# Kernel optimization log

Measured on AMD Instinct MI355X. Metric: run time of the kernel, lower is better.

The kernel has to match this reference:

```python
import jax, jax.numpy as jnp
import numpy as np

B, S, DIM = 2, 2048, 2048
N_HEADS, N_KV_HEADS = 16, 4
HEAD_DIM = DIM // N_HEADS  # 128
N_REP = N_HEADS // N_KV_HEADS  # 4


def setup_inputs() -> dict:
    key = jax.random.key(0)
    ks = jax.random.split(key, 7)
    x = jax.random.normal(ks[0], (B, S, DIM), dtype=jnp.float32)
    cos = jax.random.uniform(ks[1], (S, HEAD_DIM // 2), dtype=jnp.float32)
    sin = jax.random.uniform(ks[2], (S, HEAD_DIM // 2), dtype=jnp.float32)
    sc = 1.0 / np.sqrt(DIM)
    wq = jax.random.normal(ks[3], (DIM, N_HEADS * HEAD_DIM), dtype=jnp.float32) * sc
    wk = jax.random.normal(ks[4], (DIM, N_KV_HEADS * HEAD_DIM), dtype=jnp.float32) * sc
    wv = jax.random.normal(ks[5], (DIM, N_KV_HEADS * HEAD_DIM), dtype=jnp.float32) * sc
    wo = jax.random.normal(ks[6], (N_HEADS * HEAD_DIM, DIM), dtype=jnp.float32) * sc
    return {"x": x, "cos": cos, "sin": sin, "wq": wq, "wk": wk, "wv": wv, "wo": wo}


def _rope(t, cos, sin):
    # t: [B, S, H, hd]; cos/sin: [S, hd/2] -> broadcast as [1, S, 1, hd/2]
    tr, ti = t[..., ::2], t[..., 1::2]
    c = cos[None, :, None, :]
    s = sin[None, :, None, :]
    out_r = tr * c - ti * s
    out_i = tr * s + ti * c
    # interleave back: stack on new last axis then flatten
    return jnp.stack([out_r, out_i], axis=-1).reshape(t.shape)


def reference(x, cos, sin, wq, wk, wv, wo):
    bsz, seqlen, _ = x.shape
    xq = (x @ wq).reshape(bsz, seqlen, N_HEADS, HEAD_DIM)
    xk = (x @ wk).reshape(bsz, seqlen, N_KV_HEADS, HEAD_DIM)
    xv = (x @ wv).reshape(bsz, seqlen, N_KV_HEADS, HEAD_DIM)
    xq = _rope(xq, cos, sin)
    xk = _rope(xk, cos, sin)
    # GQA: repeat kv heads -> [B, S, H, hd]
    xk = jnp.repeat(xk, N_REP, axis=2)
    xv = jnp.repeat(xv, N_REP, axis=2)
    scale = 1.0 / jnp.sqrt(jnp.asarray(HEAD_DIM, dtype=x.dtype))
    scores = jnp.einsum("bqhd,bkhd->bhqk", xq, xk) * scale
    causal = jnp.tril(jnp.ones((seqlen, seqlen), dtype=bool))
    scores = jnp.where(causal[None, None, :, :], scores, jnp.asarray(-jnp.inf, dtype=scores.dtype))
    attn = jax.nn.softmax(scores, axis=-1)
    out = jnp.einsum("bhqk,bkhd->bqhd", attn, xv)
    out = out.reshape(bsz, seqlen, N_HEADS * HEAD_DIM)
    return out @ wo
```

## Files before the change

### kernel.cpp

```cpp
#include <hip/hip_runtime.h>
#include <stdint.h>

#define SEQ 2048

typedef uint16_t u16;
typedef uint32_t u32;
typedef __attribute__((ext_vector_type(4))) float f32x4;
typedef __attribute__((ext_vector_type(8))) __bf16 bf16x8;
typedef __attribute__((ext_vector_type(4))) __bf16 bf16x4;

__device__ __forceinline__ u16 f2bf(float f) {
    u32 u = __float_as_uint(f);
    u += 0x7FFFu + ((u >> 16) & 1u);
    return (u16)(u >> 16);
}
__device__ __forceinline__ float bf2f(u16 h) {
    return __uint_as_float(((u32)h) << 16);
}
__device__ __forceinline__ void async16(const void* g, void* l) {
    auto gp = (__attribute__((address_space(1))) void*)const_cast<void*>(g);
    auto lp = (__attribute__((address_space(3))) void*)l;
    __builtin_amdgcn_global_load_lds(gp, lp, 16, 0, 0);
}

__global__ __launch_bounds__(256) void convert_bf16(const float* __restrict__ src,
                                                    u16* __restrict__ dst) {
    int i = blockIdx.x * 256 + threadIdx.x;
    float4 v = ((const float4*)src)[i];
    u32 lo = (u32)f2bf(v.x) | ((u32)f2bf(v.y) << 16);
    u32 hi = (u32)f2bf(v.z) | ((u32)f2bf(v.w) << 16);
    ((uint2*)dst)[i] = make_uint2(lo, hi);
}

__global__ __launch_bounds__(256) void tconv_all(const float* __restrict__ wq,
                                                 const float* __restrict__ wk,
                                                 const float* __restrict__ wv,
                                                 const float* __restrict__ wo,
                                                 u16* __restrict__ wqkvT,
                                                 u16* __restrict__ woT) {
    __shared__ float tile[64][65];
    const int bx = blockIdx.x, k0 = blockIdx.y * 64;
    const float* src; u16* dst; int N, n0;
    if (bx < 32)      { src = wq; dst = wqkvT;                        N = 2048; n0 = bx * 64; }
    else if (bx < 40) { src = wk; dst = wqkvT + (size_t)2048 * 2048;  N = 512;  n0 = (bx - 32) * 64; }
    else if (bx < 48) { src = wv; dst = wqkvT + (size_t)2560 * 2048;  N = 512;  n0 = (bx - 40) * 64; }
    else              { src = wo; dst = woT;                          N = 2048; n0 = (bx - 48) * 64; }
    const int tid = threadIdx.x;
#pragma unroll
    for (int p = 0; p < 4; p++) {
        int r = p * 16 + (tid >> 4);
        int c = (tid & 15) * 4;
        float4 v = *(const float4*)&src[(size_t)(k0 + r) * N + n0 + c];
        tile[r][c] = v.x; tile[r][c+1] = v.y; tile[r][c+2] = v.z; tile[r][c+3] = v.w;
    }
    __syncthreads();
#pragma unroll
    for (int p = 0; p < 4; p++) {
        int n = p * 16 + (tid >> 4);
        int kq = (tid & 15) * 4;
        u32 lo = (u32)f2bf(tile[kq+0][n]) | ((u32)f2bf(tile[kq+1][n]) << 16);
        u32 hi = (u32)f2bf(tile[kq+2][n]) | ((u32)f2bf(tile[kq+3][n]) << 16);
        *(uint2*)&dst[(size_t)(n0 + n) * 2048 + k0 + kq] = make_uint2(lo, hi);
    }
}

template <int BN, bool F32OUT>
__global__ __launch_bounds__(512, 2) void gemm256(const u16* __restrict__ A,
                                                  const u16* __restrict__ Bt,
                                                  void* __restrict__ Cv,
                                                  int N, int K, int nbx) {
    constexpr int MF = (BN == 256) ? 8 : 4;
    constexpr int SLOT = 8192 + BN * 32;
    __shared__ u16 lds[4 * SLOT];

    const int nwg = gridDim.x;
    const int q = nwg >> 3, r = nwg & 7;
    const int xcd = blockIdx.x & 7, lid = blockIdx.x >> 3;
    const int wg = (xcd < r ? xcd * (q + 1) : r * (q + 1) + (xcd - r) * q) + lid;
    const int by = wg / nbx, bx = wg - by * nbx;
    const int m0 = by * 256, n0 = bx * BN;

    const int tid = threadIdx.x;
    const int w = tid >> 6, l = tid & 63;
    const int lr = l & 15, quad = l >> 4;
    const int wm = (BN == 256) ? (w >> 2) * 128 : (w >> 1) * 64;
    const int wn = (BN == 256) ? (w & 3) * 64  : (w & 1) * 64;
    const int cs = (quad ^ (lr & 3)) * 8;

    const int rA = w * 32 + (l >> 2);
    const int gA = ((l & 3) ^ (rA & 3)) * 8;
    const u16* aS = A + (size_t)(m0 + rA) * K + gA;
    u16* ldA = lds + (w * 128 + l) * 8;

    const u16* bS;
    u16* ldB;
    if constexpr (BN == 256) {
        bS = Bt + (size_t)(n0 + rA) * K + gA;
        ldB = lds + 8192 + (w * 128 + l) * 8;
    } else {
        const int rB = w * 16 + (l >> 2);
        const int gB = ((l & 3) ^ (rB & 3)) * 8;
        bS = Bt + (size_t)(n0 + rB) * K + gB;
        ldB = lds + 8192 + tid * 8;
    }

    f32x4 acc[MF][4] = {};
    const int nK = K >> 5;

    auto stageA = [&](int kt) {
        u16* d = ldA + (kt & 3) * SLOT;
        const u16* s = aS + (size_t)kt * 32;
        async16(s, d);
        async16(s + (size_t)16 * K, d + 512);
    };
    auto stageB = [&](int kt) {
        u16* d = ldB + (kt & 3) * SLOT;
        const u16* s = bS + (size_t)kt * 32;
        async16(s, d);
        if constexpr (BN == 256) async16(s + (size_t)16 * K, d + 512);
    };

    stageA(0); stageB(0); stageA(1); stageB(1); stageA(2); stageB(2);
    if constexpr (BN == 256)
        asm volatile("s_waitcnt vmcnt(8)" ::: "memory");
    else
        asm volatile("s_waitcnt vmcnt(6)" ::: "memory");
    __builtin_amdgcn_s_barrier();

    for (int kt = 0; kt < nK; ++kt) {
        const u16* As = lds + (kt & 3) * SLOT;
        const u16* Bs = As + 8192;
        const bool pre = (kt + 3 < nK);
        bf16x8 af[MF], bfr[4];
#pragma unroll
        for (int i = 0; i < MF; i++)
            af[i] = *(const bf16x8*)&As[(wm + i * 16 + lr) * 32 + cs];
#pragma unroll
        for (int i = 0; i < 4; i++)
            bfr[i] = *(const bf16x8*)&Bs[(wn + i * 16 + lr) * 32 + cs];
        if (pre) { stageA(kt + 3); stageB(kt + 3); }
        __builtin_amdgcn_s_barrier();
        asm volatile("s_waitcnt lgkmcnt(0)" ::: "memory");
        __builtin_amdgcn_s_setprio(1);
#pragma unroll
        for (int mf = 0; mf < MF; mf++)
#pragma unroll
            for (int nf = 0; nf < 4; nf++)
                acc[mf][nf] = __builtin_amdgcn_mfma_f32_16x16x32_bf16(af[mf], bfr[nf], acc[mf][nf], 0, 0, 0);
        __builtin_amdgcn_s_setprio(0);
        if constexpr (BN == 256) {
            if (kt < nK - 3)       asm volatile("s_waitcnt vmcnt(8)" ::: "memory");
            else if (kt == nK - 3) asm volatile("s_waitcnt vmcnt(4)" ::: "memory");
            else if (kt == nK - 2) asm volatile("s_waitcnt vmcnt(0)" ::: "memory");
        } else {
            if (kt < nK - 3)       asm volatile("s_waitcnt vmcnt(6)" ::: "memory");
            else if (kt == nK - 3) asm volatile("s_waitcnt vmcnt(3)" ::: "memory");
            else if (kt == nK - 2) asm volatile("s_waitcnt vmcnt(0)" ::: "memory");
        }
        if (kt < nK - 1) __builtin_amdgcn_s_barrier();
    }

#pragma unroll
    for (int mf = 0; mf < MF; mf++) {
#pragma unroll
        for (int nf = 0; nf < 4; nf++) {
#pragma unroll
            for (int rr = 0; rr < 4; rr++) {
                size_t row = (size_t)(m0 + wm + mf * 16 + quad * 4 + rr);
                size_t col = (size_t)(n0 + wn + nf * 16 + lr);
                if (F32OUT)
                    ((float*)Cv)[row * (size_t)N + col] = acc[mf][nf][rr];
                else
                    ((u16*)Cv)[row * (size_t)N + col] = f2bf(acc[mf][nf][rr]);
            }
        }
    }
}

__global__ __launch_bounds__(256) void rope_k(u16* __restrict__ qkv,
                                              const float* __restrict__ cosp,
                                              const float* __restrict__ sinp) {
    const int t = blockIdx.x;
    const int spos = t & (SEQ - 1);
    const int tid = threadIdx.x;
    u16* row = qkv + (size_t)t * 3072;
    const int col = 2048 + 2 * tid;
    const int ci = tid & 63;
    u32 v = *(u32*)(row + col);
    float tr = bf2f((u16)(v & 0xFFFFu));
    float ti = bf2f((u16)(v >> 16));
    float cs = cosp[spos * 64 + ci];
    float sn = sinp[spos * 64 + ci];
    float orr = tr * cs - ti * sn;
    float oi  = tr * sn + ti * cs;
    *(u32*)(row + col) = (u32)f2bf(orr) | ((u32)f2bf(oi) << 16);
}

__global__ __launch_bounds__(256) void transpose_v(const u16* __restrict__ qkv,
                                                   u16* __restrict__ vt) {
    __shared__ u16 tile[64][65];
    const int bid = blockIdx.x;
    const int dt = bid & 1;
    const int st = (bid >> 1) & 31;
    const int kh = (bid >> 6) & 3;
    const int b  = bid >> 8;
    const int tid = threadIdx.x;
#pragma unroll
    for (int pp = 0; pp < 2; pp++) {
        int r  = pp * 32 + (tid >> 3);
        int c8 = (tid & 7) * 8;
        const u16* src = qkv + (size_t)(b * SEQ + st * 64 + r) * 3072 + 2560 + kh * 128 + dt * 64 + c8;
        uint4 v = *(const uint4*)src;
        tile[r][c8+0] = (u16)(v.x & 0xFFFF); tile[r][c8+1] = (u16)(v.x >> 16);
        tile[r][c8+2] = (u16)(v.y & 0xFFFF); tile[r][c8+3] = (u16)(v.y >> 16);
        tile[r][c8+4] = (u16)(v.z & 0xFFFF); tile[r][c8+5] = (u16)(v.z >> 16);
        tile[r][c8+6] = (u16)(v.w & 0xFFFF); tile[r][c8+7] = (u16)(v.w >> 16);
    }
    __syncthreads();
#pragma unroll
    for (int pp = 0; pp < 2; pp++) {
        int dr = pp * 32 + (tid >> 3);
        int s8 = (tid & 7) * 8;
        uint4 o;
        o.x = (u32)tile[s8+0][dr] | ((u32)tile[s8+1][dr] << 16);
        o.y = (u32)tile[s8+2][dr] | ((u32)tile[s8+3][dr] << 16);
        o.z = (u32)tile[s8+4][dr] | ((u32)tile[s8+5][dr] << 16);
        o.w = (u32)tile[s8+6][dr] | ((u32)tile[s8+7][dr] << 16);
        u16* dst = vt + ((size_t)((b * 4 + kh) * 128 + dt * 64 + dr)) * SEQ + st * 64 + s8;
        *(uint4*)dst = o;
    }
}

__global__ __launch_bounds__(512, 2) void flash_attn(const u16* __restrict__ qkv,
                                                     const u16* __restrict__ vt,
                                                     const float* __restrict__ cosp,
                                                     const float* __restrict__ sinp,
                                                     u16* __restrict__ ob) {
    __shared__ u16 sh[65536];
    const int bidx = blockIdx.x;
    const int xcd   = bidx & 7;
    const int inner = bidx >> 3;
    const int b  = xcd >> 2, kh = xcd & 3;
    const int h  = kh * 4 + (inner & 3);
    const int a  = inner >> 2;
    const int tid = threadIdx.x;
    const int w = tid >> 6, lane = tid & 63;
    const int grp = w >> 2, wl = w & 3;
    const int lr = lane & 15, quad = lane >> 4;
    const float qscale = 0.088388347762f * 1.4426950408889634f;

    u16* base_g = sh + grp * 24576;
    u16* vb  = base_g + 16384;
    u16* lPw = sh + 49152 + w * 2048;

    const int tidg = tid & 255;
    const int krow = tidg >> 4;
    const int kchunk = (tidg & 15) ^ krow;
    const int vrow = tidg >> 3;
    const int vchunk = (tidg & 7) ^ (vrow & 7);
    const u16* kRow = qkv + (size_t)b * SEQ * 3072 + 2048 + kh * 128
                    + (size_t)krow * 3072 + kchunk * 8;
    const u16* vRow = vt + (size_t)(b * 4 + kh) * 128 * SEQ
                    + (size_t)vrow * SEQ + vchunk * 8;

    auto stageK = [&](int kt, int buf) {
        u16* d = base_g + buf * 8192 + tidg * 8;
#pragma unroll
        for (int i = 0; i < 4; i++)
            async16(kRow + (size_t)(kt * 64 + i * 16) * 3072, d + i * 2048);
    };
    auto stageV = [&](int kt) {
        u16* d = vb + tidg * 8;
#pragma unroll
        for (int i = 0; i < 4; i++)
            async16(vRow + (size_t)(i * 32) * SEQ + kt * 64, d + i * 2048);
    };

    float* mO = (float*)sh;
    float* mM = (float*)(sh + 49152);

    for (int p = 0; p < 2; p++) {
        const int qt = p ? (7 - a) : (8 + a);
        const int niters = p ? (8 - a) : (9 + a);
        const int kt0 = grp * niters;

        stageK(kt0, 0);

        bf16x8 qf[2][4];
#pragma unroll
        for (int qi = 0; qi < 2; qi++) {
            const int token = qt * 128 + wl * 32 + qi * 16 + lr;
            const u16* qb = qkv + (size_t)(b * SEQ + token) * 3072 + h * 128;
#pragma unroll
            for (int kk = 0; kk < 4; kk++) {
                uint4 raw = *(const uint4*)(qb + kk * 32 + quad * 8);
                u32 rw[4] = {raw.x, raw.y, raw.z, raw.w};
                union { u16 us[8]; bf16x8 v; } fr;
#pragma unroll
                for (int pp = 0; pp < 4; pp++) {
                    int ci = kk * 16 + quad * 4 + pp;
                    float cv = cosp[token * 64 + ci];
                    float sv = sinp[token * 64 + ci];
                    float tr = bf2f((u16)(rw[pp] & 0xFFFFu));
                    float ti = bf2f((u16)(rw[pp] >> 16));
                    fr.us[2 * pp]     = f2bf((tr * cv - ti * sv) * qscale);
                    fr.us[2 * pp + 1] = f2bf((tr * sv + ti * cv) * qscale);
                }
                qf[qi][kk] = fr.v;
            }
        }

        f32x4 o[2][8] = {};
        float m_st[2] = {-1e30f, -1e30f};
        float l_st[2] = {0.f, 0.f};
        const int qg = qt * 128 + wl * 32 + lr;

        for (int t = 0; t < niters; t++) {
            const int kt = kt0 + t;
            const int buf = t & 1;
            stageV(kt);
            if (t + 1 < niters) {
                stageK(kt + 1, buf ^ 1);
                asm volatile("s_waitcnt vmcnt(8)" ::: "memory");
            } else {
                asm volatile("s_waitcnt vmcnt(4)" ::: "memory");
            }
            asm volatile("s_barrier" ::: "memory");

            const u16* kcur = base_g + buf * 8192;
            f32x4 sc[2][4] = {};
            __builtin_amdgcn_s_setprio(1);
#pragma unroll
            for (int nf = 0; nf < 4; nf++) {
#pragma unroll
                for (int kk = 0; kk < 4; kk++) {
                    bf16x8 ak = *(const bf16x8*)&kcur[(nf * 16 + lr) * 128 + (((kk * 4 + quad) ^ lr) * 8)];
                    sc[0][nf] = __builtin_amdgcn_mfma_f32_16x16x32_bf16(ak, qf[0][kk], sc[0][nf], 0, 0, 0);
                    sc[1][nf] = __builtin_amdgcn_mfma_f32_16x16x32_bf16(ak, qf[1][kk], sc[1][nf], 0, 0, 0);
                }
            }
            __builtin_amdgcn_s_setprio(0);

            const int kb = kt * 64 + quad * 4;
            const int kmax = kt * 64 + 63;
#pragma unroll
            for (int qi = 0; qi < 2; qi++) {
                float ps[4][4];
                float tmax = -1e30f;
                const int qrow_g = qg + qi * 16;
                if (kmax > qt * 128 + wl * 32 + qi * 16) {
#pragma unroll
                    for (int nf = 0; nf < 4; nf++)
#pragma unroll
                        for (int r = 0; r < 4; r++) {
                            float v = sc[qi][nf][r];
                            if ((kb + nf * 16 + r) > qrow_g) v = -1e30f;
                            ps[nf][r] = v;
                            tmax = fmaxf(tmax, v);
                        }
                } else {
#pragma unroll
                    for (int nf = 0; nf < 4; nf++)
#pragma unroll
                        for (int r = 0; r < 4; r++) {
                            float v = sc[qi][nf][r];
                            ps[nf][r] = v;
                            tmax = fmaxf(tmax, v);
                        }
                }
                tmax = fmaxf(tmax, __shfl_xor(tmax, 16));
                tmax = fmaxf(tmax, __shfl_xor(tmax, 32));
                const float mprev = m_st[qi];
                if (!__all(tmax - mprev <= 8.0f)) {
                    float mnew = fmaxf(mprev, tmax);
                    float alpha = exp2f(mprev - mnew);
                    l_st[qi] *= alpha;
                    m_st[qi] = mnew;
#pragma unroll
                    for (int r = 0; r < 4; r++) {
                        float ar = __shfl(alpha, quad * 4 + r, 16);
#pragma unroll
                        for (int nd = 0; nd < 8; nd++) o[qi][nd][r] *= ar;
                    }
                }
                const float mcur = m_st[qi];
                float rsum = 0.f;
#pragma unroll
                for (int nf = 0; nf < 4; nf++)
#pragma unroll
                    for (int r = 0; r < 4; r++) {
                        float e = exp2f(ps[nf][r] - mcur);
                        ps[nf][r] = e;
                        rsum += e;
                    }
                rsum += __shfl_xor(rsum, 16);
                rsum += __shfl_xor(rsum, 32);
                l_st[qi] += rsum;
                const int qrow = qi * 16 + lr;
#pragma unroll
                for (int nf = 0; nf < 4; nf++) {
                    u32 lo = (u32)f2bf(ps[nf][0]) | ((u32)f2bf(ps[nf][1]) << 16);
                    u32 hi = (u32)f2bf(ps[nf][2]) | ((u32)f2bf(ps[nf][3]) << 16);
                    int c = (nf * 4 + quad) ^ lr;
                    *(uint2*)&lPw[qrow * 64 + c * 4] = make_uint2(lo, hi);
                }
            }

            if (t + 1 < niters) asm volatile("s_waitcnt vmcnt(4)" ::: "memory");
            else                asm volatile("s_waitcnt vmcnt(0)" ::: "memory");
            asm volatile("s_barrier" ::: "memory");

            __builtin_amdgcn_s_setprio(1);
#pragma unroll
            for (int kf = 0; kf < 2; kf++) {
                bf16x8 pa[2];
#pragma unroll
                for (int qi = 0; qi < 2; qi++) {
                    int c0 = (kf * 8 + quad * 2) ^ lr;
                    int c1 = (kf * 8 + quad * 2 + 1) ^ lr;
                    bf16x4 p0 = *(const bf16x4*)&lPw[(qi * 16 + lr) * 64 + c0 * 4];
                    bf16x4 p1 = *(const bf16x4*)&lPw[(qi * 16 + lr) * 64 + c1 * 4];
                    pa[qi] = __builtin_shufflevector(p0, p1, 0, 1, 2, 3, 4, 5, 6, 7);
                }
#pragma unroll
                for (int nd = 0; nd < 8; nd++) {
                    bf16x8 vv = *(const bf16x8*)&vb[(nd * 16 + lr) * 64 + (((kf * 4 + quad) ^ (lr & 7)) * 8)];
                    o[0][nd] = __builtin_amdgcn_mfma_f32_16x16x32_bf16(pa[0], vv, o[0][nd], 0, 0, 0);
                    o[1][nd] = __builtin_amdgcn_mfma_f32_16x16x32_bf16(pa[1], vv, o[1][nd], 0, 0, 0);
                }
            }
            __builtin_amdgcn_s_setprio(0);

            asm volatile("s_barrier" ::: "memory");
        }

        __syncthreads();
        if (grp == 1) {
#pragma unroll
            for (int qi = 0; qi < 2; qi++) {
#pragma unroll
                for (int r = 0; r < 4; r++) {
                    int row = wl * 32 + qi * 16 + quad * 4 + r;
#pragma unroll
                    for (int nd = 0; nd < 8; nd++)
                        mO[row * 128 + nd * 16 + lr] = o[qi][nd][r];
                }
                if (quad == 0) {
                    int rowl = wl * 32 + qi * 16 + lr;
                    mM[rowl * 2]     = m_st[qi];
                    mM[rowl * 2 + 1] = l_st[qi];
                }
            }
        }
        __syncthreads();
        if (grp == 0) {
#pragma unroll
            for (int qi = 0; qi < 2; qi++) {
                int rowl = wl * 32 + qi * 16 + lr;
                float m1 = mM[rowl * 2], l1 = mM[rowl * 2 + 1];
                float M  = fmaxf(m_st[qi], m1);
                float a0 = exp2f(m_st[qi] - M);
                float a1 = exp2f(m1 - M);
                float li = 1.0f / (l_st[qi] * a0 + l1 * a1);
                u16* obase = ob + (size_t)(b * SEQ + qt * 128 + wl * 32 + qi * 16) * 2048 + h * 128;
#pragma unroll
                for (int r = 0; r < 4; r++) {
                    float a0b = __shfl(a0, quad * 4 + r, 16);
                    float a1b = __shfl(a1, quad * 4 + r, 16);
                    float lib = __shfl(li, quad * 4 + r, 16);
                    int row = wl * 32 + qi * 16 + quad * 4 + r;
#pragma unroll
                    for (int nd = 0; nd < 8; nd++) {
                        float val = (o[qi][nd][r] * a0b + mO[row * 128 + nd * 16 + lr] * a1b) * lib;
                        obase[(quad * 4 + r) * 2048 + nd * 16 + lr] = f2bf(val);
                    }
                }
            }
        }
        __syncthreads();
    }
}

extern "C" void kernel_launch(void* const* d_in, const int* in_sizes, int n_in,
                              void* d_out, int out_size, void* d_ws, size_t ws_size,
                              hipStream_t stream) {
    (void)in_sizes; (void)n_in; (void)out_size; (void)ws_size;
    const float* x    = (const float*)d_in[0];
    const float* cosp = (const float*)d_in[1];
    const float* sinp = (const float*)d_in[2];
    const float* wq   = (const float*)d_in[3];
    const float* wk   = (const float*)d_in[4];
    const float* wv   = (const float*)d_in[5];
    const float* wo   = (const float*)d_in[6];
    float* out = (float*)d_out;

    char* ws = (char*)d_ws;
    u16* xb    = (u16*)(ws);
    u16* qkvb  = (u16*)(ws + (size_t)16 * 1024 * 1024);
    u16* wqkvT = (u16*)(ws + (size_t)40 * 1024 * 1024);
    u16* woT   = (u16*)(ws + (size_t)52 * 1024 * 1024);
    u16* vtb   = (u16*)(ws + (size_t)60 * 1024 * 1024);
    u16* ob    = xb;

    convert_bf16<<<8192, 256, 0, stream>>>(x, xb);
    tconv_all<<<dim3(80, 32), 256, 0, stream>>>(wq, wk, wv, wo, wqkvT, woT);
    gemm256<256, false><<<192, 512, 0, stream>>>(xb, wqkvT, (void*)qkvb, 3072, 2048, 12);
    rope_k<<<4096, 256, 0, stream>>>(qkvb, cosp, sinp);
    transpose_v<<<512, 256, 0, stream>>>(qkvb, vtb);
    flash_attn<<<256, 512, 0, stream>>>(qkvb, vtb, cosp, sinp, ob);
    gemm256<128, true><<<256, 512, 0, stream>>>(ob, woT, (void*)out, 2048, 2048, 16);
}
```

Before: 316.4 us.

## Fuse K RoPE and V transpose into QKV GEMM epilogue, split GEMM k-loop

Removes the separate rope_k and transpose_v kernels. The QKV GEMM epilogue now applies RoPE to the K columns, using a lane shuffle to fetch the pair partner, and writes V directly in transposed layout. The BN=256 GEMM main loop is split into two half-M phases that interleave the A and B prefetch with MFMA work. Manual bf16 rounding is replaced with the packed v_cvt_pk_bf16_f32 instruction, and the softmax max/sum reductions are split into independent chains. This saves two kernel launches and a round trip of K and V through memory, at the cost of extra barriers in the GEMM loop and scattered, uncoalesced global loads of cos/sin in the epilogue.

```diff
diff --git a/kernel.cpp b/kernel.cpp
--- a/kernel.cpp
+++ b/kernel.cpp
@@ -17,6 +17,11 @@
 __device__ __forceinline__ float bf2f(u16 h) {
     return __uint_as_float(((u32)h) << 16);
 }
+__device__ __forceinline__ u32 cvt_pk_bf16(float lo, float hi) {
+    u32 r;
+    asm("v_cvt_pk_bf16_f32 %0, %1, %2" : "=v"(r) : "v"(lo), "v"(hi));
+    return r;
+}
 __device__ __forceinline__ void async16(const void* g, void* l) {
     auto gp = (__attribute__((address_space(1))) void*)const_cast<void*>(g);
     auto lp = (__attribute__((address_space(3))) void*)l;
@@ -27,9 +32,7 @@
                                                     u16* __restrict__ dst) {
     int i = blockIdx.x * 256 + threadIdx.x;
     float4 v = ((const float4*)src)[i];
-    u32 lo = (u32)f2bf(v.x) | ((u32)f2bf(v.y) << 16);
-    u32 hi = (u32)f2bf(v.z) | ((u32)f2bf(v.w) << 16);
-    ((uint2*)dst)[i] = make_uint2(lo, hi);
+    ((uint2*)dst)[i] = make_uint2(cvt_pk_bf16(v.x, v.y), cvt_pk_bf16(v.z, v.w));
 }
 
 __global__ __launch_bounds__(256) void tconv_all(const float* __restrict__ wq,
@@ -58,8 +61,8 @@
     for (int p = 0; p < 4; p++) {
         int n = p * 16 + (tid >> 4);
         int kq = (tid & 15) * 4;
-        u32 lo = (u32)f2bf(tile[kq+0][n]) | ((u32)f2bf(tile[kq+1][n]) << 16);
-        u32 hi = (u32)f2bf(tile[kq+2][n]) | ((u32)f2bf(tile[kq+3][n]) << 16);
+        u32 lo = cvt_pk_bf16(tile[kq+0][n], tile[kq+1][n]);
+        u32 hi = cvt_pk_bf16(tile[kq+2][n], tile[kq+3][n]);
         *(uint2*)&dst[(size_t)(n0 + n) * 2048 + k0 + kq] = make_uint2(lo, hi);
     }
 }
@@ -68,7 +71,10 @@
 __global__ __launch_bounds__(512, 2) void gemm256(const u16* __restrict__ A,
                                                   const u16* __restrict__ Bt,
                                                   void* __restrict__ Cv,
-                                                  int N, int K, int nbx) {
+                                                  int N, int K, int nbx,
+                                                  const float* __restrict__ cosp,
+                                                  const float* __restrict__ sinp,
+                                                  u16* __restrict__ vt) {
     constexpr int MF = (BN == 256) ? 8 : 4;
     constexpr int SLOT = 8192 + BN * 32;
     __shared__ u16 lds[4 * SLOT];
@@ -131,103 +137,129 @@
         const u16* As = lds + (kt & 3) * SLOT;
         const u16* Bs = As + 8192;
         const bool pre = (kt + 3 < nK);
-        bf16x8 af[MF], bfr[4];
-#pragma unroll
-        for (int i = 0; i < MF; i++)
-            af[i] = *(const bf16x8*)&As[(wm + i * 16 + lr) * 32 + cs];
-#pragma unroll
-        for (int i = 0; i < 4; i++)
-            bfr[i] = *(const bf16x8*)&Bs[(wn + i * 16 + lr) * 32 + cs];
-        if (pre) { stageA(kt + 3); stageB(kt + 3); }
-        __builtin_amdgcn_s_barrier();
-        asm volatile("s_waitcnt lgkmcnt(0)" ::: "memory");
-        __builtin_amdgcn_s_setprio(1);
-#pragma unroll
-        for (int mf = 0; mf < MF; mf++)
-#pragma unroll
-            for (int nf = 0; nf < 4; nf++)
-                acc[mf][nf] = __builtin_amdgcn_mfma_f32_16x16x32_bf16(af[mf], bfr[nf], acc[mf][nf], 0, 0, 0);
-        __builtin_amdgcn_s_setprio(0);
         if constexpr (BN == 256) {
+            bf16x8 af[4], bfr[4];
+#pragma unroll
+            for (int i = 0; i < 4; i++)
+                af[i] = *(const bf16x8*)&As[(wm + i * 16 + lr) * 32 + cs];
+#pragma unroll
+            for (int i = 0; i < 4; i++)
+                bfr[i] = *(const bf16x8*)&Bs[(wn + i * 16 + lr) * 32 + cs];
+            if (pre) stageA(kt + 3);
+            __builtin_amdgcn_s_barrier();
+            asm volatile("s_waitcnt lgkmcnt(0)" ::: "memory");
+            __builtin_amdgcn_s_setprio(1);
+#pragma unroll
+            for (int mf = 0; mf < 4; mf++)
+#pragma unroll
+                for (int nf = 0; nf < 4; nf++)
+                    acc[mf][nf] = __builtin_amdgcn_mfma_f32_16x16x32_bf16(af[mf], bfr[nf], acc[mf][nf], 0, 0, 0);
+            __builtin_amdgcn_s_setprio(0);
+            __builtin_amdgcn_s_barrier();
+#pragma unroll
+            for (int i = 0; i < 4; i++)
+                af[i] = *(const bf16x8*)&As[(wm + 64 + i * 16 + lr) * 32 + cs];
+            if (pre) stageB(kt + 3);
+            __builtin_amdgcn_s_barrier();
+            asm volatile("s_waitcnt lgkmcnt(0)" ::: "memory");
+            __builtin_amdgcn_s_setprio(1);
+#pragma unroll
+            for (int mf = 0; mf < 4; mf++)
+#pragma unroll
+                for (int nf = 0; nf < 4; nf++)
+                    acc[4 + mf][nf] = __builtin_amdgcn_mfma_f32_16x16x32_bf16(af[mf], bfr[nf], acc[4 + mf][nf], 0, 0, 0);
+            __builtin_amdgcn_s_setprio(0);
             if (kt < nK - 3)       asm volatile("s_waitcnt vmcnt(8)" ::: "memory");
             else if (kt == nK - 3) asm volatile("s_waitcnt vmcnt(4)" ::: "memory");
             else if (kt == nK - 2) asm volatile("s_waitcnt vmcnt(0)" ::: "memory");
+            if (kt < nK - 1) __builtin_amdgcn_s_barrier();
         } else {
+            bf16x8 af[MF], bfr[4];
+#pragma unroll
+            for (int i = 0; i < MF; i++)
+                af[i] = *(const bf16x8*)&As[(wm + i * 16 + lr) * 32 + cs];
+#pragma unroll
+            for (int i = 0; i < 4; i++)
+                bfr[i] = *(const bf16x8*)&Bs[(wn + i * 16 + lr) * 32 + cs];
+            if (pre) { stageA(kt + 3); stageB(kt + 3); }
+            __builtin_amdgcn_s_barrier();
+            asm volatile("s_waitcnt lgkmcnt(0)" ::: "memory");
+            __builtin_amdgcn_s_setprio(1);
+#pragma unroll
+            for (int mf = 0; mf < MF; mf++)
+#pragma unroll
+                for (int nf = 0; nf < 4; nf++)
+                    acc[mf][nf] = __builtin_amdgcn_mfma_f32_16x16x32_bf16(af[mf], bfr[nf], acc[mf][nf], 0, 0, 0);
+            __builtin_amdgcn_s_setprio(0);
             if (kt < nK - 3)       asm volatile("s_waitcnt vmcnt(6)" ::: "memory");
             else if (kt == nK - 3) asm volatile("s_waitcnt vmcnt(3)" ::: "memory");
             else if (kt == nK - 2) asm volatile("s_waitcnt vmcnt(0)" ::: "memory");
-        }
-        if (kt < nK - 1) __builtin_amdgcn_s_barrier();
-    }
-
-#pragma unroll
-    for (int mf = 0; mf < MF; mf++) {
-#pragma unroll
-        for (int nf = 0; nf < 4; nf++) {
-#pragma unroll
-            for (int rr = 0; rr < 4; rr++) {
-                size_t row = (size_t)(m0 + wm + mf * 16 + quad * 4 + rr);
-                size_t col = (size_t)(n0 + wn + nf * 16 + lr);
-                if (F32OUT)
-                    ((float*)Cv)[row * (size_t)N + col] = acc[mf][nf][rr];
-                else
-                    ((u16*)Cv)[row * (size_t)N + col] = f2bf(acc[mf][nf][rr]);
-            }
+            if (kt < nK - 1) __builtin_amdgcn_s_barrier();
         }
     }
-}
-
-__global__ __launch_bounds__(256) void rope_k(u16* __restrict__ qkv,
-                                              const float* __restrict__ cosp,
-                                              const float* __restrict__ sinp) {
-    const int t = blockIdx.x;
-    const int spos = t & (SEQ - 1);
-    const int tid = threadIdx.x;
-    u16* row = qkv + (size_t)t * 3072;
-    const int col = 2048 + 2 * tid;
-    const int ci = tid & 63;
-    u32 v = *(u32*)(row + col);
-    float tr = bf2f((u16)(v & 0xFFFFu));
-    float ti = bf2f((u16)(v >> 16));
-    float cs = cosp[spos * 64 + ci];
-    float sn = sinp[spos * 64 + ci];
-    float orr = tr * cs - ti * sn;
-    float oi  = tr * sn + ti * cs;
-    *(u32*)(row + col) = (u32)f2bf(orr) | ((u32)f2bf(oi) << 16);
-}
-
-__global__ __launch_bounds__(256) void transpose_v(const u16* __restrict__ qkv,
-                                                   u16* __restrict__ vt) {
-    __shared__ u16 tile[64][65];
-    const int bid = blockIdx.x;
-    const int dt = bid & 1;
-    const int st = (bid >> 1) & 31;
-    const int kh = (bid >> 6) & 3;
-    const int b  = bid >> 8;
-    const int tid = threadIdx.x;
-#pragma unroll
-    for (int pp = 0; pp < 2; pp++) {
-        int r  = pp * 32 + (tid >> 3);
-        int c8 = (tid & 7) * 8;
-        const u16* src = qkv + (size_t)(b * SEQ + st * 64 + r) * 3072 + 2560 + kh * 128 + dt * 64 + c8;
-        uint4 v = *(const uint4*)src;
-        tile[r][c8+0] = (u16)(v.x & 0xFFFF); tile[r][c8+1] = (u16)(v.x >> 16);
-        tile[r][c8+2] = (u16)(v.y & 0xFFFF); tile[r][c8+3] = (u16)(v.y >> 16);
-        tile[r][c8+4] = (u16)(v.z & 0xFFFF); tile[r][c8+5] = (u16)(v.z >> 16);
-        tile[r][c8+6] = (u16)(v.w & 0xFFFF); tile[r][c8+7] = (u16)(v.w >> 16);
-    }
-    __syncthreads();
-#pragma unroll
-    for (int pp = 0; pp < 2; pp++) {
-        int dr = pp * 32 + (tid >> 3);
-        int s8 = (tid & 7) * 8;
-        uint4 o;
-        o.x = (u32)tile[s8+0][dr] | ((u32)tile[s8+1][dr] << 16);
-        o.y = (u32)tile[s8+2][dr] | ((u32)tile[s8+3][dr] << 16);
-        o.z = (u32)tile[s8+4][dr] | ((u32)tile[s8+5][dr] << 16);
-        o.w = (u32)tile[s8+6][dr] | ((u32)tile[s8+7][dr] << 16);
-        u16* dst = vt + ((size_t)((b * 4 + kh) * 128 + dt * 64 + dr)) * SEQ + st * 64 + s8;
-        *(uint4*)dst = o;
+
+    if constexpr (BN == 256 && !F32OUT) {
+        if (n0 >= 2560) {
+            const int bb = m0 >> 11;
+#pragma unroll
+            for (int mf = 0; mf < MF; mf++) {
+                const int token0 = (m0 + wm + mf * 16 + quad * 4) & (SEQ - 1);
+#pragma unroll
+                for (int nf = 0; nf < 4; nf++) {
+                    int dg = n0 - 2560 + wn + nf * 16 + lr;
+                    int kh = dg >> 7, d = dg & 127;
+                    u32 lo = cvt_pk_bf16(acc[mf][nf][0], acc[mf][nf][1]);
+                    u32 hi = cvt_pk_bf16(acc[mf][nf][2], acc[mf][nf][3]);
+                    *(uint2*)&vt[((size_t)((bb * 4 + kh) * 128 + d)) * SEQ + token0] = make_uint2(lo, hi);
+                }
+            }
+        } else if (n0 >= 2048) {
+            const float sgn = (lr & 1) ? 1.0f : -1.0f;
+#pragma unroll
+            for (int mf = 0; mf < MF; mf++) {
+#pragma unroll
+                for (int nf = 0; nf < 4; nf++) {
+                    int col = n0 + wn + nf * 16 + lr;
+                    int ci = (col & 127) >> 1;
+#pragma unroll
+                    for (int rr = 0; rr < 4; rr++) {
+                        size_t row = (size_t)(m0 + wm + mf * 16 + quad * 4 + rr);
+                        int token = (int)row & (SEQ - 1);
+                        float v = acc[mf][nf][rr];
+                        float ppart = __shfl_xor(v, 1);
+                        float c = cosp[token * 64 + ci];
+                        float s = sinp[token * 64 + ci];
+                        float ov = fmaf(sgn * ppart, s, v * c);
+                        ((u16*)Cv)[row * (size_t)N + col] = f2bf(ov);
+                    }
+                }
+            }
+        } else {
+#pragma unroll
+            for (int mf = 0; mf < MF; mf++)
+#pragma unroll
+                for (int nf = 0; nf < 4; nf++)
+#pragma unroll
+                    for (int rr = 0; rr < 4; rr++) {
+                        size_t row = (size_t)(m0 + wm + mf * 16 + quad * 4 + rr);
+                        size_t col = (size_t)(n0 + wn + nf * 16 + lr);
+                        ((u16*)Cv)[row * (size_t)N + col] = f2bf(acc[mf][nf][rr]);
+                    }
+        }
+    } else {
+#pragma unroll
+        for (int mf = 0; mf < MF; mf++)
+#pragma unroll
+            for (int nf = 0; nf < 4; nf++)
+#pragma unroll
+                for (int rr = 0; rr < 4; rr++) {
+                    size_t row = (size_t)(m0 + wm + mf * 16 + quad * 4 + rr);
+                    size_t col = (size_t)(n0 + wn + nf * 16 + lr);
+                    if (F32OUT)
+                        ((float*)Cv)[row * (size_t)N + col] = acc[mf][nf][rr];
+                    else
+                        ((u16*)Cv)[row * (size_t)N + col] = f2bf(acc[mf][nf][rr]);
+                }
     }
 }
 
@@ -295,7 +327,7 @@
             for (int kk = 0; kk < 4; kk++) {
                 uint4 raw = *(const uint4*)(qb + kk * 32 + quad * 8);
                 u32 rw[4] = {raw.x, raw.y, raw.z, raw.w};
-                union { u16 us[8]; bf16x8 v; } fr;
+                union { u32 u[4]; bf16x8 v; } fr;
 #pragma unroll
                 for (int pp = 0; pp < 4; pp++) {
                     int ci = kk * 16 + quad * 4 + pp;
@@ -303,8 +335,8 @@
                     float sv = sinp[token * 64 + ci];
                     float tr = bf2f((u16)(rw[pp] & 0xFFFFu));
                     float ti = bf2f((u16)(rw[pp] >> 16));
-                    fr.us[2 * pp]     = f2bf((tr * cv - ti * sv) * qscale);
-                    fr.us[2 * pp + 1] = f2bf((tr * sv + ti * cv) * qscale);
+                    fr.u[pp] = cvt_pk_bf16((tr * cv - ti * sv) * qscale,
+                                           (tr * sv + ti * cv) * qscale);
                 }
                 qf[qi][kk] = fr.v;
             }
@@ -346,28 +378,33 @@
 #pragma unroll
             for (int qi = 0; qi < 2; qi++) {
                 float ps[4][4];
-                float tmax = -1e30f;
+                float tm[4];
                 const int qrow_g = qg + qi * 16;
                 if (kmax > qt * 128 + wl * 32 + qi * 16) {
 #pragma unroll
-                    for (int nf = 0; nf < 4; nf++)
+                    for (int nf = 0; nf < 4; nf++) {
+                        tm[nf] = -1e30f;
 #pragma unroll
                         for (int r = 0; r < 4; r++) {
                             float v = sc[qi][nf][r];
                             if ((kb + nf * 16 + r) > qrow_g) v = -1e30f;
                             ps[nf][r] = v;
-                            tmax = fmaxf(tmax, v);
+                            tm[nf] = fmaxf(tm[nf], v);
                         }
+                    }
                 } else {
 #pragma unroll
-                    for (int nf = 0; nf < 4; nf++)
+                    for (int nf = 0; nf < 4; nf++) {
+                        tm[nf] = -1e30f;
 #pragma unroll
                         for (int r = 0; r < 4; r++) {
                             float v = sc[qi][nf][r];
                             ps[nf][r] = v;
-                            tmax = fmaxf(tmax, v);
+                            tm[nf] = fmaxf(tm[nf], v);
                         }
-                }
+                    }
+                }
+                float tmax = fmaxf(fmaxf(tm[0], tm[1]), fmaxf(tm[2], tm[3]));
                 tmax = fmaxf(tmax, __shfl_xor(tmax, 16));
                 tmax = fmaxf(tmax, __shfl_xor(tmax, 32));
                 const float mprev = m_st[qi];
@@ -384,23 +421,26 @@
                     }
                 }
                 const float mcur = m_st[qi];
-                float rsum = 0.f;
-#pragma unroll
-                for (int nf = 0; nf < 4; nf++)
+                float rs[4];
+#pragma unroll
+                for (int nf = 0; nf < 4; nf++) {
+                    rs[nf] = 0.f;
 #pragma unroll
                     for (int r = 0; r < 4; r++) {
                         float e = exp2f(ps[nf][r] - mcur);
                         ps[nf][r] = e;
-                        rsum += e;
-                    }
+                        rs[nf] += e;
+                    }
+                }
+                float rsum = (rs[0] + rs[1]) + (rs[2] + rs[3]);
                 rsum += __shfl_xor(rsum, 16);
                 rsum += __shfl_xor(rsum, 32);
                 l_st[qi] += rsum;
                 const int qrow = qi * 16 + lr;
 #pragma unroll
                 for (int nf = 0; nf < 4; nf++) {
-                    u32 lo = (u32)f2bf(ps[nf][0]) | ((u32)f2bf(ps[nf][1]) << 16);
-                    u32 hi = (u32)f2bf(ps[nf][2]) | ((u32)f2bf(ps[nf][3]) << 16);
+                    u32 lo = cvt_pk_bf16(ps[nf][0], ps[nf][1]);
+                    u32 hi = cvt_pk_bf16(ps[nf][2], ps[nf][3]);
                     int c = (nf * 4 + quad) ^ lr;
                     *(uint2*)&lPw[qrow * 64 + c * 4] = make_uint2(lo, hi);
                 }
@@ -504,9 +544,9 @@
 
     convert_bf16<<<8192, 256, 0, stream>>>(x, xb);
     tconv_all<<<dim3(80, 32), 256, 0, stream>>>(wq, wk, wv, wo, wqkvT, woT);
-    gemm256<256, false><<<192, 512, 0, stream>>>(xb, wqkvT, (void*)qkvb, 3072, 2048, 12);
-    rope_k<<<4096, 256, 0, stream>>>(qkvb, cosp, sinp);
-    transpose_v<<<512, 256, 0, stream>>>(qkvb, vtb);
+    gemm256<256, false><<<192, 512, 0, stream>>>(xb, wqkvT, (void*)qkvb, 3072, 2048, 12,
+                                                 cosp, sinp, vtb);
     flash_attn<<<256, 512, 0, stream>>>(qkvb, vtb, cosp, sinp, ob);
-    gemm256<128, true><<<256, 512, 0, stream>>>(ob, woT, (void*)out, 2048, 2048, 16);
-}
+    gemm256<128, true><<<256, 512, 0, stream>>>(ob, woT, (void*)out, 2048, 2048, 16,
+                                                nullptr, nullptr, nullptr);
+}
```

Result: no change. 317.9 us (+0.5%).
